# Optimization experiments

Hardware: AMD Instinct MI355X
Metric: run time of the kernel (lower is better)

## Reference

```python
import jax, jax.numpy as jnp
import numpy as np

B, C, L, DEG = 64, 2, 4096, 4  # batch, n_classes, n_labels, max children (4-ary tree)


def setup_inputs() -> dict:
    key = jax.random.key(0)
    k1, k2 = jax.random.split(key)
    emissions = jax.random.normal(k1, (B, C, L), dtype=jnp.float32)
    transitions = jax.random.normal(k2, (L, L, C, C), dtype=jnp.float32)
    # deterministic 4-ary tree: children of j are 4j+1..4j+4 (if < L)
    succ_idx = np.zeros((L, DEG), dtype=np.int32)
    succ_mask = np.zeros((L, DEG), dtype=bool)
    for j in range(L):
        ch = [4 * j + 1 + d for d in range(DEG) if 4 * j + 1 + d < L]
        succ_idx[j, : len(ch)] = ch
        succ_mask[j, : len(ch)] = True
    order = np.arange(L, dtype=np.int32)  # parents before children -> valid topo order
    return {
        "emissions": emissions,
        "transitions": transitions,
        "succ_idx": jnp.asarray(succ_idx),
        "succ_mask": jnp.asarray(succ_mask),
        "order": jnp.asarray(order),
    }


def reference(emissions, transitions, succ_idx, succ_mask, order):
    # Sequential tree DP: for each node j (topological order), send
    # logsumexp-combined messages to its successors. Ragged successor lists
    # are padded to DEG with a mask; masked slots contribute exactly 0,
    # matching the original `if successors.size(0) > 0` skip.
    def step(messages, j):
        idx = succ_idx[j]            # [D] padded successor indices
        mask = succ_mask[j]          # [D]
        local = emissions[:, :, j] + messages[:, :, j]          # [B, C]
        trans = transitions[idx, j]                             # [D, C, C]
        # elem[d, c_succ, b, c_j] = local[b, c_j] + trans[d, c_succ, c_j]
        elem = local[None, None, :, :] + trans[:, :, None, :]   # [D, C, B, C]
        m = jax.scipy.special.logsumexp(elem, axis=3)           # [D, C, B]
        contrib = jnp.where(mask[:, None, None], m, 0.0).transpose(2, 1, 0)  # [B, C, D]
        return messages.at[:, :, idx].add(contrib), None

    messages0 = jnp.zeros_like(emissions)
    messages, _ = jax.lax.scan(step, messages0, order)
    return messages
```

## Files before the change

kernel.cpp:

```cpp
#include <hip/hip_runtime.h>
#include <math.h>


#define LL 4096
#define BB 64

__device__ __forceinline__ float lse2(float a, float b) {
    float hi = fmaxf(a, b);
    float lo = fminf(a, b);
    return hi + __logf(1.0f + __expf(lo - hi));
}

__global__ __launch_bounds__(256) void mp_chain_kernel(
    const float* __restrict__ emis,
    const float* __restrict__ trans,
    float* __restrict__ out)
{
    int tid = blockIdx.x * blockDim.x + threadIdx.x;
    int b = tid >> 12;
    int j = tid & (LL - 1);
    const float* eb = emis + (size_t)b * 2 * LL;
    float* ob = out + (size_t)b * 2 * LL;

    if (j == 0) {
        ob[0] = 0.0f;
        ob[LL] = 0.0f;
        return;
    }

    const int S[7] = {0, 1, 5, 21, 85, 341, 1365};
    int l = 1 + (j >= 5) + (j >= 21) + (j >= 85) + (j >= 341) + (j >= 1365);
    int o = j - S[l];

    float m0 = 0.0f, m1 = 0.0f;
    int prev = 0;
#pragma unroll
    for (int k = 1; k <= 6; ++k) {
        if (k > l) break;
        int cur = S[k] + (o >> (2 * (l - k)));
        float l0 = eb[prev] + m0;
        float l1 = eb[LL + prev] + m1;
        const float4 t = *(const float4*)(trans + (((size_t)cur * LL + prev) << 2));
        m0 = lse2(l0 + t.x, l1 + t.y);
        m1 = lse2(l0 + t.z, l1 + t.w);
        prev = cur;
    }

    ob[j] = m0;
    ob[LL + j] = m1;
}

extern "C" void kernel_launch(void* const* d_in, const int* in_sizes, int n_in,
                              void* d_out, int out_size, void* d_ws, size_t ws_size,
                              hipStream_t stream) {
    const float* emis  = (const float*)d_in[0];
    const float* trans = (const float*)d_in[1];
    float* out = (float*)d_out;
    const int total = BB * LL;
    mp_chain_kernel<<<total / 256, 256, 0, stream>>>(emis, trans, out);
}
```

Before: 302.9 us.

## Pre-gather tree edge transitions into a compact buffer and make chain loop branchless

Adds a pre-pass kernel that gathers the 4096 parent-child transition float4s out of the huge sparse transitions tensor into a dense workspace array. The main kernel then reads edges from this compact, cache-friendly buffer instead of scattered strided locations. The per-level loop is also made uniform across the wave: every thread runs all six steps, with predicated updates and the level offsets computed by bit masks instead of a lookup table. This costs an extra kernel launch and redundant lse work for shallow nodes.

```diff
diff --git a/kernel.cpp b/kernel.cpp
--- a/kernel.cpp
+++ b/kernel.cpp
@@ -11,43 +11,51 @@
     return hi + __logf(1.0f + __expf(lo - hi));
 }
 
+__global__ __launch_bounds__(256) void compact_edges(
+    const float* __restrict__ trans, float4* __restrict__ edge)
+{
+    int j = blockIdx.x * 256 + threadIdx.x;
+    if (j == 0) { edge[0] = make_float4(0.f, 0.f, 0.f, 0.f); return; }
+    int p = (j - 1) >> 2;
+    edge[j] = *(const float4*)(trans + (((size_t)j * LL + p) << 2));
+}
+
 __global__ __launch_bounds__(256) void mp_chain_kernel(
     const float* __restrict__ emis,
-    const float* __restrict__ trans,
+    const float4* __restrict__ edge,
     float* __restrict__ out)
 {
     int tid = blockIdx.x * blockDim.x + threadIdx.x;
     int b = tid >> 12;
     int j = tid & (LL - 1);
     const float* eb = emis + (size_t)b * 2 * LL;
-    float* ob = out + (size_t)b * 2 * LL;
 
-    if (j == 0) {
-        ob[0] = 0.0f;
-        ob[LL] = 0.0f;
-        return;
-    }
+    int l = (j >= 1) + (j >= 5) + (j >= 21) + (j >= 85) + (j >= 341) + (j >= 1365);
+    unsigned Sl = 0x55555555u & ((1u << (2 * l)) - 1u);
+    int o = j - (int)Sl;
+    int shift = 6 - l;
 
-    const int S[7] = {0, 1, 5, 21, 85, 341, 1365};
-    int l = 1 + (j >= 5) + (j >= 21) + (j >= 85) + (j >= 341) + (j >= 1365);
-    int o = j - S[l];
-
-    float m0 = 0.0f, m1 = 0.0f;
+    float m0 = 0.f, m1 = 0.f;
     int prev = 0;
 #pragma unroll
-    for (int k = 1; k <= 6; ++k) {
-        if (k > l) break;
-        int cur = S[k] + (o >> (2 * (l - k)));
-        float l0 = eb[prev] + m0;
-        float l1 = eb[LL + prev] + m1;
-        const float4 t = *(const float4*)(trans + (((size_t)cur * LL + prev) << 2));
-        m0 = lse2(l0 + t.x, l1 + t.y);
-        m1 = lse2(l0 + t.z, l1 + t.w);
+    for (int s = 1; s <= 6; ++s) {
+        bool active = (s > shift);
+        int k = s - shift; if (k < 1) k = 1;
+        unsigned Sk = 0x55555555u & ((1u << (2 * k)) - 1u);
+        int cur = active ? (int)(Sk + (unsigned)(o >> (2 * (6 - s)))) : 0;
+        float4 t = edge[cur];
+        float e0 = eb[prev];
+        float e1 = eb[LL + prev];
+        float l0 = e0 + m0, l1 = e1 + m1;
+        float n0 = lse2(l0 + t.x, l1 + t.y);
+        float n1 = lse2(l0 + t.z, l1 + t.w);
+        m0 = active ? n0 : m0;
+        m1 = active ? n1 : m1;
         prev = cur;
     }
 
-    ob[j] = m0;
-    ob[LL + j] = m1;
+    out[(size_t)b * 2 * LL + j]      = m0;
+    out[(size_t)b * 2 * LL + LL + j] = m1;
 }
 
 extern "C" void kernel_launch(void* const* d_in, const int* in_sizes, int n_in,
@@ -56,6 +64,8 @@
     const float* emis  = (const float*)d_in[0];
     const float* trans = (const float*)d_in[1];
     float* out = (float*)d_out;
-    const int total = BB * LL;
-    mp_chain_kernel<<<total / 256, 256, 0, stream>>>(emis, trans, out);
+    float4* edge = (float4*)d_ws;
+
+    compact_edges<<<LL / 256, 256, 0, stream>>>(trans, edge);
+    mp_chain_kernel<<<(BB * LL) / 256, 256, 0, stream>>>(emis, edge, out);
 }
```

After: 303.1 us. About the same (+0.1%).
